# Kernel tuning notes

Hardware: AMD Instinct MI355X
Metric: run time of the kernel (lower is better)

The kernel has to match this reference:

```python
import jax, jax.numpy as jnp
import numpy as np

N_NODES = 50000
N_EDGES = 400000
V = 3        # view_num
D = 128      # per-view input width (nfeat / view_num)
H = 128      # nhid


def setup_inputs() -> dict:
    key = jax.random.key(0)
    k_h, k_src, k_dst, k_w1, k_w2 = jax.random.split(key, 5)
    h = jax.random.normal(k_h, (N_NODES, V * D), dtype=jnp.float32)
    src = jax.random.randint(k_src, (N_EDGES,), 0, N_NODES, dtype=jnp.int32)
    dst = jax.random.randint(k_dst, (N_EDGES,), 0, N_NODES, dtype=jnp.int32)
    s1 = 1.0 / np.sqrt(D)
    s2 = 1.0 / np.sqrt(H)
    W1 = jax.random.uniform(k_w1, (V, D, H), dtype=jnp.float32, minval=-s1, maxval=s1)
    b1 = jnp.zeros((V, H), dtype=jnp.float32)
    W2 = jax.random.uniform(k_w2, (H, H), dtype=jnp.float32, minval=-s2, maxval=s2)
    b2 = jnp.zeros((H,), dtype=jnp.float32)
    return {"h": h, "src": src, "dst": dst, "W1": W1, "b1": b1, "W2": W2, "b2": b2}


def _agg(x, src, dst, n_nodes):
    # DGL GraphConv(norm='none') aggregation: out[d] = sum_{(s->d) in E} x[s]
    return jax.ops.segment_sum(x[src], dst, num_segments=n_nodes)


def reference(h, src, dst, W1, b1, W2, b2):
    n = h.shape[0]
    x = h.reshape(n, V, D)  # split into views along feature dim
    # layer 1 (per-view GraphConv + relu):  relu( A @ (x_v W1_v) + b1_v )
    xw = jnp.einsum('nvd,vdh->nvh', x, W1)
    y = jax.nn.relu(_agg(xw, src, dst, n) + b1)
    # dropout p=0 / eval mode -> identity
    # layer 2 (shared GraphConv + relu)
    yw = jnp.einsum('nvh,hk->nvk', y, W2)
    z = jax.nn.relu(_agg(yw, src, dst, n) + b2)
    # agg_type=0 -> plain concat of views
    return z.reshape(n, V * H)
```

## Files before the change

kernel.cpp:

```cpp
#include <hip/hip_runtime.h>

constexpr int NN = 50000;
constexpr int NE = 400000;
constexpr int NV = 3;
constexpr int DF = 128;
constexpr int F  = 384;
constexpr int TR = 32;
constexpr int NB = (NN + 255) / 256;
constexpr int SP = 136;

typedef short  bf16x8 __attribute__((ext_vector_type(8)));
typedef float  f32x4  __attribute__((ext_vector_type(4)));


__global__ void k_count(const int* __restrict__ dst, int* __restrict__ deg) {
  int i = blockIdx.x * blockDim.x + threadIdx.x;
  int stride = gridDim.x * blockDim.x;
  for (int e = i; e < NE; e += stride) atomicAdd(&deg[dst[e]], 1);
}

__global__ void k_blocksum(const int* __restrict__ deg, int* __restrict__ bsum) {
  __shared__ int s[4];
  int i = blockIdx.x * 256 + threadIdx.x;
  int v = (i < NN) ? deg[i] : 0;
  for (int o = 32; o > 0; o >>= 1) v += __shfl_down(v, o);
  if ((threadIdx.x & 63) == 0) s[threadIdx.x >> 6] = v;
  __syncthreads();
  if (threadIdx.x == 0) bsum[blockIdx.x] = s[0] + s[1] + s[2] + s[3];
}

__global__ void k_scanb(int* __restrict__ bsum, int nb, int* __restrict__ offs_n) {
  if (threadIdx.x == 0 && blockIdx.x == 0) {
    int run = 0;
    for (int i = 0; i < nb; ++i) { int v = bsum[i]; bsum[i] = run; run += v; }
    *offs_n = run;
  }
}

__global__ void k_offsets(const int* __restrict__ deg, const int* __restrict__ bsum,
                          int* __restrict__ offs, int* __restrict__ cur) {
  __shared__ int s[256];
  int t = threadIdx.x;
  int i = blockIdx.x * 256 + t;
  int v = (i < NN) ? deg[i] : 0;
  s[t] = v;
  __syncthreads();
  for (int o = 1; o < 256; o <<= 1) {
    int add = (t >= o) ? s[t - o] : 0;
    __syncthreads();
    s[t] += add;
    __syncthreads();
  }
  if (i < NN) {
    offs[i] = bsum[blockIdx.x] + s[t] - v;
    cur[i] = 0;
  }
}

__global__ void k_scatter(const int* __restrict__ src, const int* __restrict__ dst,
                          const int* __restrict__ offs, int* __restrict__ cnt,
                          int* __restrict__ csr) {
  int i = blockIdx.x * blockDim.x + threadIdx.x;
  int stride = gridDim.x * blockDim.x;
  for (int e = i; e < NE; e += stride) {
    int d = dst[e];
    int pos = offs[d] + atomicAdd(&cnt[d], 1);
    csr[pos] = src[e];
  }
}


__device__ __forceinline__ ushort f2bf(float f) {
  unsigned u = __float_as_uint(f);
  u = (u + 0x7fffu + ((u >> 16) & 1u)) >> 16;
  return (ushort)u;
}

__global__ void k_tobf16(const float* __restrict__ in, ushort* __restrict__ outb, int n4) {
  int i = blockIdx.x * blockDim.x + threadIdx.x;
  int stride = gridDim.x * blockDim.x;
  const float4* in4 = (const float4*)in;
  for (int k = i; k < n4; k += stride) {
    float4 x = in4[k];
    ushort4 u;
    u.x = f2bf(x.x); u.y = f2bf(x.y); u.z = f2bf(x.z); u.w = f2bf(x.w);
    *(ushort4*)(outb + (size_t)k * 4) = u;
  }
}

__global__ void k_wprep(const float* __restrict__ W, ushort* __restrict__ pk, int nv) {
  int idx = blockIdx.x * 256 + threadIdx.x;
  if (idx >= nv * 2 * 16384) return;
  int j = idx & 7, lane = (idx >> 3) & 63, cb = (idx >> 9) & 7, kb = (idx >> 12) & 3;
  int vs = idx >> 14;
  int v = vs >> 1, s = vs & 1;
  int d = kb * 32 + (lane >> 4) * 8 + j;
  int c = cb * 16 + (lane & 15);
  float w = W[((size_t)v * DF + d) * DF + c];
  ushort hi = f2bf(w);
  ushort outv = hi;
  if (s) {
    float rem = w - __uint_as_float((unsigned)hi << 16);
    outv = f2bf(rem);
  }
  pk[idx] = outv;
}


template <bool OUT_BF16>
__global__ __launch_bounds__(256, 4)
void k_layer(const ushort* __restrict__ feat,
             const int* __restrict__ offs, const int* __restrict__ csr,
             const ushort* __restrict__ Wpk, int vmul,
             const float* __restrict__ ball, int bstride,
             void* __restrict__ outp) {
  __shared__ ushort sThi[TR][SP];
  __shared__ ushort sTlo[TR][SP];
  const int t = threadIdx.x;
  const int v = blockIdx.y;
  const float* __restrict__ bias = ball + (size_t)v * bstride;

  const int wave = t >> 6, lane = t & 63;
  const int lane15 = lane & 15, lgrp = lane >> 4;
  const int row0 = blockIdx.x * TR;
  const int vcol = v * DF + lane * 2;
  const int lane2 = lane * 2;

#pragma unroll
  for (int rr = 0; rr < TR / 4; ++rr) {
    int r = rr * 4 + wave;
    int node = row0 + r;
    float ax = 0.f, ay = 0.f;
    if (node < NN) {
      int e0 = offs[node], e1 = offs[node + 1];
      int e = e0;
      while (e < e1) {
        int n = e1 - e; if (n > 64) n = 64;
        int ce = e + lane; if (ce > e1 - 1) ce = e1 - 1;
        int idx = csr[ce];
        int j = 0;
        for (; j + 8 <= n; j += 8) {
          int s0 = __builtin_amdgcn_readlane(idx, j);
          int s1 = __builtin_amdgcn_readlane(idx, j + 1);
          int s2 = __builtin_amdgcn_readlane(idx, j + 2);
          int s3 = __builtin_amdgcn_readlane(idx, j + 3);
          int s4 = __builtin_amdgcn_readlane(idx, j + 4);
          int s5 = __builtin_amdgcn_readlane(idx, j + 5);
          int s6 = __builtin_amdgcn_readlane(idx, j + 6);
          int s7 = __builtin_amdgcn_readlane(idx, j + 7);
          unsigned u0 = *(const unsigned*)(feat + (size_t)s0 * F + vcol);
          unsigned u1 = *(const unsigned*)(feat + (size_t)s1 * F + vcol);
          unsigned u2 = *(const unsigned*)(feat + (size_t)s2 * F + vcol);
          unsigned u3 = *(const unsigned*)(feat + (size_t)s3 * F + vcol);
          unsigned u4 = *(const unsigned*)(feat + (size_t)s4 * F + vcol);
          unsigned u5 = *(const unsigned*)(feat + (size_t)s5 * F + vcol);
          unsigned u6 = *(const unsigned*)(feat + (size_t)s6 * F + vcol);
          unsigned u7 = *(const unsigned*)(feat + (size_t)s7 * F + vcol);
          ax += __uint_as_float(u0 << 16); ay += __uint_as_float(u0 & 0xffff0000u);
          ax += __uint_as_float(u1 << 16); ay += __uint_as_float(u1 & 0xffff0000u);
          ax += __uint_as_float(u2 << 16); ay += __uint_as_float(u2 & 0xffff0000u);
          ax += __uint_as_float(u3 << 16); ay += __uint_as_float(u3 & 0xffff0000u);
          ax += __uint_as_float(u4 << 16); ay += __uint_as_float(u4 & 0xffff0000u);
          ax += __uint_as_float(u5 << 16); ay += __uint_as_float(u5 & 0xffff0000u);
          ax += __uint_as_float(u6 << 16); ay += __uint_as_float(u6 & 0xffff0000u);
          ax += __uint_as_float(u7 << 16); ay += __uint_as_float(u7 & 0xffff0000u);
        }
        if (j + 4 <= n) {
          int s0 = __builtin_amdgcn_readlane(idx, j);
          int s1 = __builtin_amdgcn_readlane(idx, j + 1);
          int s2 = __builtin_amdgcn_readlane(idx, j + 2);
          int s3 = __builtin_amdgcn_readlane(idx, j + 3);
          unsigned u0 = *(const unsigned*)(feat + (size_t)s0 * F + vcol);
          unsigned u1 = *(const unsigned*)(feat + (size_t)s1 * F + vcol);
          unsigned u2 = *(const unsigned*)(feat + (size_t)s2 * F + vcol);
          unsigned u3 = *(const unsigned*)(feat + (size_t)s3 * F + vcol);
          ax += __uint_as_float(u0 << 16); ay += __uint_as_float(u0 & 0xffff0000u);
          ax += __uint_as_float(u1 << 16); ay += __uint_as_float(u1 & 0xffff0000u);
          ax += __uint_as_float(u2 << 16); ay += __uint_as_float(u2 & 0xffff0000u);
          ax += __uint_as_float(u3 << 16); ay += __uint_as_float(u3 & 0xffff0000u);
          j += 4;
        }
        for (; j < n; ++j) {
          int s0 = __builtin_amdgcn_readlane(idx, j);
          unsigned u0 = *(const unsigned*)(feat + (size_t)s0 * F + vcol);
          ax += __uint_as_float(u0 << 16); ay += __uint_as_float(u0 & 0xffff0000u);
        }
        e += n;
      }
    }
    ushort hx = f2bf(ax);
    ushort lx = f2bf(ax - __uint_as_float((unsigned)hx << 16));
    ushort hy = f2bf(ay);
    ushort ly = f2bf(ay - __uint_as_float((unsigned)hy << 16));
    *(unsigned*)&sThi[r][lane2] = (unsigned)hx | ((unsigned)hy << 16);
    *(unsigned*)&sTlo[r][lane2] = (unsigned)lx | ((unsigned)ly << 16);
  }
  __syncthreads();

  const ushort* pkbase = Wpk + (size_t)(v * vmul) * (2 * 4 * 8 * 512);
  const float bv0 = bias[wave * 32 + lane15];
  const float bv1 = bias[wave * 32 + 16 + lane15];
  f32x4 acc00 = {bv0, bv0, bv0, bv0};
  f32x4 acc01 = {bv1, bv1, bv1, bv1};
  f32x4 acc10 = {bv0, bv0, bv0, bv0};
  f32x4 acc11 = {bv1, bv1, bv1, bv1};

#pragma unroll
  for (int kb = 0; kb < 4; ++kb) {
    const int acol = kb * 32 + lgrp * 8;
    bf16x8 ah0 = *(const bf16x8*)&sThi[lane15][acol];
    bf16x8 ah1 = *(const bf16x8*)&sThi[16 + lane15][acol];
    bf16x8 al0 = *(const bf16x8*)&sTlo[lane15][acol];
    bf16x8 al1 = *(const bf16x8*)&sTlo[16 + lane15][acol];
    bf16x8 bh0 = *(const bf16x8*)(pkbase + ((size_t)((0 * 4 + kb) * 8 + wave * 2 + 0)) * 512 + lane * 8);
    bf16x8 bh1 = *(const bf16x8*)(pkbase + ((size_t)((0 * 4 + kb) * 8 + wave * 2 + 1)) * 512 + lane * 8);
    bf16x8 bl0 = *(const bf16x8*)(pkbase + ((size_t)((1 * 4 + kb) * 8 + wave * 2 + 0)) * 512 + lane * 8);
    bf16x8 bl1 = *(const bf16x8*)(pkbase + ((size_t)((1 * 4 + kb) * 8 + wave * 2 + 1)) * 512 + lane * 8);
    acc00 = __builtin_amdgcn_mfma_f32_16x16x32_bf16(ah0, bh0, acc00, 0, 0, 0);
    acc00 = __builtin_amdgcn_mfma_f32_16x16x32_bf16(al0, bh0, acc00, 0, 0, 0);
    acc00 = __builtin_amdgcn_mfma_f32_16x16x32_bf16(ah0, bl0, acc00, 0, 0, 0);
    acc01 = __builtin_amdgcn_mfma_f32_16x16x32_bf16(ah0, bh1, acc01, 0, 0, 0);
    acc01 = __builtin_amdgcn_mfma_f32_16x16x32_bf16(al0, bh1, acc01, 0, 0, 0);
    acc01 = __builtin_amdgcn_mfma_f32_16x16x32_bf16(ah0, bl1, acc01, 0, 0, 0);
    acc10 = __builtin_amdgcn_mfma_f32_16x16x32_bf16(ah1, bh0, acc10, 0, 0, 0);
    acc10 = __builtin_amdgcn_mfma_f32_16x16x32_bf16(al1, bh0, acc10, 0, 0, 0);
    acc10 = __builtin_amdgcn_mfma_f32_16x16x32_bf16(ah1, bl0, acc10, 0, 0, 0);
    acc11 = __builtin_amdgcn_mfma_f32_16x16x32_bf16(ah1, bh1, acc11, 0, 0, 0);
    acc11 = __builtin_amdgcn_mfma_f32_16x16x32_bf16(al1, bh1, acc11, 0, 0, 0);
    acc11 = __builtin_amdgcn_mfma_f32_16x16x32_bf16(ah1, bl1, acc11, 0, 0, 0);
  }

  const int colbase = v * DF + wave * 32 + lane15;
#pragma unroll
  for (int rb = 0; rb < 2; ++rb) {
    f32x4 a0 = rb ? acc10 : acc00;
    f32x4 a1 = rb ? acc11 : acc01;
#pragma unroll
    for (int k = 0; k < 4; ++k) {
      int row = row0 + rb * 16 + lgrp * 4 + k;
      if (row < NN) {
        float x0 = a0[k] > 0.f ? a0[k] : 0.f;
        float x1 = a1[k] > 0.f ? a1[k] : 0.f;
        if (OUT_BF16) {
          ushort* ob = (ushort*)outp;
          ob[(size_t)row * F + colbase]      = f2bf(x0);
          ob[(size_t)row * F + colbase + 16] = f2bf(x1);
        } else {
          float* of = (float*)outp;
          of[(size_t)row * F + colbase]      = x0;
          of[(size_t)row * F + colbase + 16] = x1;
        }
      }
    }
  }
}


static inline size_t align_up(size_t x, size_t a) { return (x + a - 1) & ~(a - 1); }

extern "C" void kernel_launch(void* const* d_in, const int* in_sizes, int n_in,
                              void* d_out, int out_size, void* d_ws, size_t ws_size,
                              hipStream_t stream) {
  const float* h   = (const float*)d_in[0];
  const int*   src = (const int*)d_in[1];
  const int*   dst = (const int*)d_in[2];
  const float* W1  = (const float*)d_in[3];
  const float* b1  = (const float*)d_in[4];
  const float* W2  = (const float*)d_in[5];
  const float* b2  = (const float*)d_in[6];
  float* out = (float*)d_out;

  char* ws = (char*)d_ws;
  size_t o = 0;
  int* deg  = (int*)(ws + o); o = align_up(o + (size_t)NN * 4, 1024);
  int* cur  = (int*)(ws + o); o = align_up(o + (size_t)NN * 4, 1024);
  int* offs = (int*)(ws + o); o = align_up(o + (size_t)(NN + 1) * 4, 1024);
  int* bsum = (int*)(ws + o); o = align_up(o + 1024, 1024);
  int* csr  = (int*)(ws + o); o = align_up(o + (size_t)NE * 4, 1024);
  ushort* hb   = (ushort*)(ws + o); o = align_up(o + (size_t)NN * F * 2, 1024);
  ushort* ybuf = (ushort*)(ws + o); o = align_up(o + (size_t)NN * F * 2, 1024);
  ushort* w1pk = (ushort*)(ws + o); o = align_up(o + (size_t)NV * 2 * 16384 * 2, 1024);
  ushort* w2pk = (ushort*)(ws + o); o = align_up(o + (size_t)1 * 2 * 16384 * 2, 1024);
  (void)ws_size; (void)n_in; (void)in_sizes; (void)out_size;

  hipMemsetAsync(deg, 0, (size_t)NN * 4, stream);
  k_count<<<1024, 256, 0, stream>>>(dst, deg);
  k_blocksum<<<NB, 256, 0, stream>>>(deg, bsum);
  k_scanb<<<1, 64, 0, stream>>>(bsum, NB, offs + NN);
  k_offsets<<<NB, 256, 0, stream>>>(deg, bsum, offs, cur);
  k_scatter<<<1024, 256, 0, stream>>>(src, dst, offs, cur, csr);
  k_tobf16<<<2048, 256, 0, stream>>>(h, hb, NN * F / 4);
  k_wprep<<<(NV * 2 * 16384) / 256, 256, 0, stream>>>(W1, w1pk, NV);
  k_wprep<<<(2 * 16384) / 256, 256, 0, stream>>>(W2, w2pk, 1);

  dim3 grid((NN + TR - 1) / TR, NV);
  k_layer<true ><<<grid, 256, 0, stream>>>(hb,   offs, csr, w1pk, 1, b1, DF, ybuf);
  k_layer<false><<<grid, 256, 0, stream>>>(ybuf, offs, csr, w2pk, 0, b2, 0,  out);
}
```

Baseline: 227.9 us.

## Fuse preprocessing kernels and parallelize block-sum scan

```diff
diff --git a/kernel.cpp b/kernel.cpp
--- a/kernel.cpp
+++ b/kernel.cpp
@@ -13,11 +13,63 @@
 typedef float  f32x4  __attribute__((ext_vector_type(4)));
 
 
-__global__ void k_count(const int* __restrict__ dst, int* __restrict__ deg) {
-  int i = blockIdx.x * blockDim.x + threadIdx.x;
-  int stride = gridDim.x * blockDim.x;
-  for (int e = i; e < NE; e += stride) atomicAdd(&deg[dst[e]], 1);
-}
+__device__ __forceinline__ ushort f2bf(float f) {
+  unsigned u = __float_as_uint(f);
+  u = (u + 0x7fffu + ((u >> 16) & 1u)) >> 16;
+  return (ushort)u;
+}
+
+
+__device__ __forceinline__ void wprep_one(const float* __restrict__ W,
+                                          ushort* __restrict__ pk, int idx) {
+  int j = idx & 7, lane = (idx >> 3) & 63, cb = (idx >> 9) & 7, kb = (idx >> 12) & 3;
+  int vs = idx >> 14;
+  int v = vs >> 1, s = vs & 1;
+  int d = kb * 32 + (lane >> 4) * 8 + j;
+  int c = cb * 16 + (lane & 15);
+  float w = W[((size_t)v * DF + d) * DF + c];
+  ushort hi = f2bf(w);
+  ushort outv = hi;
+  if (s) outv = f2bf(w - __uint_as_float((unsigned)hi << 16));
+  pk[idx] = outv;
+}
+
+constexpr int WB1 = (NV * 2 * 16384) / 256;
+constexpr int WB2 = (2 * 16384) / 256;
+
+__global__ void k_prep0(const float* __restrict__ W1, const float* __restrict__ W2,
+                        ushort* __restrict__ w1pk, ushort* __restrict__ w2pk,
+                        int* __restrict__ deg) {
+  int b = blockIdx.x, t = threadIdx.x;
+  if (b < WB1) {
+    wprep_one(W1, w1pk, b * 256 + t);
+  } else if (b < WB1 + WB2) {
+    wprep_one(W2, w2pk, (b - WB1) * 256 + t);
+  } else {
+    int i = (b - WB1 - WB2) * 256 + t;
+    if (i < NN) deg[i] = 0;
+  }
+}
+
+
+__global__ void k_cvtcnt(const float* __restrict__ in, ushort* __restrict__ outb,
+                         const int* __restrict__ dst, int* __restrict__ deg) {
+  int b = blockIdx.x, t = threadIdx.x;
+  if (b < 2048) {
+    const int n4 = NN * F / 4;
+    const float4* in4 = (const float4*)in;
+    for (int k = b * 256 + t; k < n4; k += 2048 * 256) {
+      float4 x = in4[k];
+      ushort4 u;
+      u.x = f2bf(x.x); u.y = f2bf(x.y); u.z = f2bf(x.z); u.w = f2bf(x.w);
+      *(ushort4*)(outb + (size_t)k * 4) = u;
+    }
+  } else {
+    for (int e = (b - 2048) * 256 + t; e < NE; e += 1024 * 256)
+      atomicAdd(&deg[dst[e]], 1);
+  }
+}
+
 
 __global__ void k_blocksum(const int* __restrict__ deg, int* __restrict__ bsum) {
   __shared__ int s[4];
@@ -29,16 +81,24 @@
   if (threadIdx.x == 0) bsum[blockIdx.x] = s[0] + s[1] + s[2] + s[3];
 }
 
-__global__ void k_scanb(int* __restrict__ bsum, int nb, int* __restrict__ offs_n) {
-  if (threadIdx.x == 0 && blockIdx.x == 0) {
-    int run = 0;
-    for (int i = 0; i < nb; ++i) { int v = bsum[i]; bsum[i] = run; run += v; }
-    *offs_n = run;
-  }
+__global__ void k_scanpar(int* __restrict__ bsum, int* __restrict__ offs_n) {
+  __shared__ int s[256];
+  int t = threadIdx.x;
+  int v = (t < NB) ? bsum[t] : 0;
+  s[t] = v;
+  __syncthreads();
+  for (int o = 1; o < 256; o <<= 1) {
+    int add = (t >= o) ? s[t - o] : 0;
+    __syncthreads();
+    s[t] += add;
+    __syncthreads();
+  }
+  if (t < NB) bsum[t] = s[t] - v;
+  if (t == NB - 1) *offs_n = s[t];
 }
 
 __global__ void k_offsets(const int* __restrict__ deg, const int* __restrict__ bsum,
-                          int* __restrict__ offs, int* __restrict__ cur) {
+                          int* __restrict__ offs) {
   __shared__ int s[256];
   int t = threadIdx.x;
   int i = blockIdx.x * 256 + t;
@@ -51,59 +111,19 @@
     s[t] += add;
     __syncthreads();
   }
-  if (i < NN) {
-    offs[i] = bsum[blockIdx.x] + s[t] - v;
-    cur[i] = 0;
-  }
+  if (i < NN) offs[i] = bsum[blockIdx.x] + s[t] - v;
 }
 
 __global__ void k_scatter(const int* __restrict__ src, const int* __restrict__ dst,
-                          const int* __restrict__ offs, int* __restrict__ cnt,
+                          const int* __restrict__ offs, int* __restrict__ deg,
                           int* __restrict__ csr) {
   int i = blockIdx.x * blockDim.x + threadIdx.x;
   int stride = gridDim.x * blockDim.x;
   for (int e = i; e < NE; e += stride) {
     int d = dst[e];
-    int pos = offs[d] + atomicAdd(&cnt[d], 1);
+    int pos = offs[d] + atomicSub(&deg[d], 1) - 1;
     csr[pos] = src[e];
   }
-}
-
-
-__device__ __forceinline__ ushort f2bf(float f) {
-  unsigned u = __float_as_uint(f);
-  u = (u + 0x7fffu + ((u >> 16) & 1u)) >> 16;
-  return (ushort)u;
-}
-
-__global__ void k_tobf16(const float* __restrict__ in, ushort* __restrict__ outb, int n4) {
-  int i = blockIdx.x * blockDim.x + threadIdx.x;
-  int stride = gridDim.x * blockDim.x;
-  const float4* in4 = (const float4*)in;
-  for (int k = i; k < n4; k += stride) {
-    float4 x = in4[k];
-    ushort4 u;
-    u.x = f2bf(x.x); u.y = f2bf(x.y); u.z = f2bf(x.z); u.w = f2bf(x.w);
-    *(ushort4*)(outb + (size_t)k * 4) = u;
-  }
-}
-
-__global__ void k_wprep(const float* __restrict__ W, ushort* __restrict__ pk, int nv) {
-  int idx = blockIdx.x * 256 + threadIdx.x;
-  if (idx >= nv * 2 * 16384) return;
-  int j = idx & 7, lane = (idx >> 3) & 63, cb = (idx >> 9) & 7, kb = (idx >> 12) & 3;
-  int vs = idx >> 14;
-  int v = vs >> 1, s = vs & 1;
-  int d = kb * 32 + (lane >> 4) * 8 + j;
-  int c = cb * 16 + (lane & 15);
-  float w = W[((size_t)v * DF + d) * DF + c];
-  ushort hi = f2bf(w);
-  ushort outv = hi;
-  if (s) {
-    float rem = w - __uint_as_float((unsigned)hi << 16);
-    outv = f2bf(rem);
-  }
-  pk[idx] = outv;
 }
 
 
@@ -273,7 +293,6 @@
   char* ws = (char*)d_ws;
   size_t o = 0;
   int* deg  = (int*)(ws + o); o = align_up(o + (size_t)NN * 4, 1024);
-  int* cur  = (int*)(ws + o); o = align_up(o + (size_t)NN * 4, 1024);
   int* offs = (int*)(ws + o); o = align_up(o + (size_t)(NN + 1) * 4, 1024);
   int* bsum = (int*)(ws + o); o = align_up(o + 1024, 1024);
   int* csr  = (int*)(ws + o); o = align_up(o + (size_t)NE * 4, 1024);
@@ -283,15 +302,12 @@
   ushort* w2pk = (ushort*)(ws + o); o = align_up(o + (size_t)1 * 2 * 16384 * 2, 1024);
   (void)ws_size; (void)n_in; (void)in_sizes; (void)out_size;
 
-  hipMemsetAsync(deg, 0, (size_t)NN * 4, stream);
-  k_count<<<1024, 256, 0, stream>>>(dst, deg);
+  k_prep0<<<WB1 + WB2 + NB, 256, 0, stream>>>(W1, W2, w1pk, w2pk, deg);
+  k_cvtcnt<<<3072, 256, 0, stream>>>(h, hb, dst, deg);
   k_blocksum<<<NB, 256, 0, stream>>>(deg, bsum);
-  k_scanb<<<1, 64, 0, stream>>>(bsum, NB, offs + NN);
-  k_offsets<<<NB, 256, 0, stream>>>(deg, bsum, offs, cur);
-  k_scatter<<<1024, 256, 0, stream>>>(src, dst, offs, cur, csr);
-  k_tobf16<<<2048, 256, 0, stream>>>(h, hb, NN * F / 4);
-  k_wprep<<<(NV * 2 * 16384) / 256, 256, 0, stream>>>(W1, w1pk, NV);
-  k_wprep<<<(2 * 16384) / 256, 256, 0, stream>>>(W2, w2pk, 1);
+  k_scanpar<<<1, 256, 0, stream>>>(bsum, offs + NN);
+  k_offsets<<<NB, 256, 0, stream>>>(deg, bsum, offs);
+  k_scatter<<<1024, 256, 0, stream>>>(src, dst, offs, deg, csr);
 
   dim3 grid((NN + TR - 1) / TR, NV);
   k_layer<true ><<<grid, 256, 0, stream>>>(hb,   offs, csr, w1pk, 1, b1, DF, ybuf);
```

Measured after the change: 203.1 us. -10.9%, faster.
